# Performance work log

Measured on AMD Instinct MI355X. Metric: run time of the kernel, lower is better.

## Reference

```python
import jax, jax.numpy as jnp
import numpy as np


def setup_inputs() -> dict:
    key = jax.random.key(0)
    k0, k1, k2, k3 = jax.random.split(key, 4)
    B, T, D, F, E = 4, 2048, 512, 1024, 8
    x = jax.random.normal(k0, (B, T, D), dtype=jnp.float32)
    # router weight is zero-init in the original; use small random values so top-k
    router_w = 0.02 * jax.random.normal(k1, (E, D), dtype=jnp.float32)
    router_b = jnp.zeros((E,), dtype=jnp.float32)
    w_gate_up = 0.02 * jax.random.normal(k2, (E, D, 2 * F), dtype=jnp.float32)
    w_down = 0.02 * jax.random.normal(k3, (E, F, D), dtype=jnp.float32)
    return {"x": x, "router_w": router_w, "router_b": router_b,
            "w_gate_up": w_gate_up, "w_down": w_down, "top_k": 2}


def reference(x, router_w, router_b, w_gate_up, w_down, top_k):
    B, T, D = x.shape
    E = router_w.shape[0]
    x_flat = x.reshape(-1, D)                      # [N, D]
    N = x_flat.shape[0]

    # router: softmax over experts, top-k, renormalize
    logits = x_flat @ router_w.T + router_b       # [N, E]
    probs = jax.nn.softmax(logits, axis=-1)
    top_w, top_idx = jax.lax.top_k(probs, top_k)  # [N, k]
    top_w = top_w / jnp.sum(top_w, axis=-1, keepdims=True)

    # scatter renormalized weights into a dense [N, E] combine matrix
    combine = jnp.zeros((N, E), dtype=x.dtype).at[
        jnp.arange(N)[:, None], top_idx].add(top_w)

    # per-expert SwiGLU; combine weights zero out non-selected experts, giving
    # math identical to the sort/gather/scatter dispatch in the original
    out = jnp.zeros_like(x_flat)
    for e in range(E):  # fixed small expert count, not a data-dim loop
        gate_up = x_flat @ w_gate_up[e]           # [N, 2F]
        gate, up = jnp.split(gate_up, 2, axis=-1)
        h = jax.nn.silu(gate) * up                # [N, F]
        out = out + combine[:, e:e + 1] * (h @ w_down[e])
    return out.reshape(B, T, D)
```

## Files before the change

kernel.cpp:

```cpp
#include <hip/hip_runtime.h>
#include <stdint.h>

#define N_TOK 8192
#define D_DIM 512
#define F_DIM 1024
#define E_NUM 8
#define M_SLOTS (N_TOK * 2)

typedef __bf16 bf16x8 __attribute__((ext_vector_type(8)));
typedef float f32x4 __attribute__((ext_vector_type(4)));

__device__ __forceinline__ ushort f2b(float f) {
    union { float f; unsigned u; } v; v.f = f;
    unsigned r = v.u + 0x7fffu + ((v.u >> 16) & 1u);
    return (ushort)(r >> 16);
}
__device__ __forceinline__ float b2f(ushort u) {
    union { unsigned i; float f; } v; v.i = ((unsigned)u) << 16; return v.f;
}
__device__ __forceinline__ void gload16(const void* g, void* l) {
    __builtin_amdgcn_global_load_lds(
        (const __attribute__((address_space(1))) unsigned int*)g,
        (__attribute__((address_space(3))) unsigned int*)l, 16, 0, 0);
}

__global__ __launch_bounds__(256) void pre_k(const float* __restrict__ x,
                                             const float* __restrict__ rw,
                                             const float* __restrict__ rb,
                                             ushort* __restrict__ x_bf,
                                             int* __restrict__ tok_e,
                                             float* __restrict__ tok_w,
                                             int* __restrict__ cnt,
                                             const float* __restrict__ wgu,
                                             ushort* __restrict__ wgu_t,
                                             const float* __restrict__ wd,
                                             ushort* __restrict__ wd_t) {
    __shared__ ushort tile[64][65];
    int b = blockIdx.x;
    if (b < N_TOK / 4) {
        if (b == 0 && threadIdx.x < 16) cnt[threadIdx.x] = 0;
        int lane = threadIdx.x & 63, wv = threadIdx.x >> 6;
        int t = b * 4 + wv;
        float4 xa = *(const float4*)(x + (size_t)t * D_DIM + lane * 8);
        float4 xb = *(const float4*)(x + (size_t)t * D_DIM + lane * 8 + 4);
        ushort u[8] = {f2b(xa.x), f2b(xa.y), f2b(xa.z), f2b(xa.w),
                       f2b(xb.x), f2b(xb.y), f2b(xb.z), f2b(xb.w)};
        *(uint4*)(x_bf + (size_t)t * D_DIM + lane * 8) = *(const uint4*)u;

        float acc[E_NUM];
#pragma unroll
        for (int e = 0; e < E_NUM; ++e) {
            float4 wa = *(const float4*)(rw + (size_t)e * D_DIM + lane * 8);
            float4 wb = *(const float4*)(rw + (size_t)e * D_DIM + lane * 8 + 4);
            float s = xa.x * wa.x + xa.y * wa.y + xa.z * wa.z + xa.w * wa.w +
                      xb.x * wb.x + xb.y * wb.y + xb.z * wb.z + xb.w * wb.w;
#pragma unroll
            for (int o = 32; o > 0; o >>= 1) s += __shfl_xor(s, o, 64);
            acc[e] = s;
        }
        if (lane == 0) {
            float l[E_NUM];
#pragma unroll
            for (int e = 0; e < E_NUM; ++e) l[e] = acc[e] + rb[e];
            int e0 = 0;
#pragma unroll
            for (int e = 1; e < E_NUM; ++e) if (l[e] > l[e0]) e0 = e;
            int e1 = (e0 == 0) ? 1 : 0;
#pragma unroll
            for (int e = 0; e < E_NUM; ++e) if (e != e0 && l[e] > l[e1]) e1 = e;
            float p1 = __expf(l[e1] - l[e0]);
            float w0 = 1.f / (1.f + p1), w1 = p1 / (1.f + p1);
            tok_e[2 * t] = e0;  tok_e[2 * t + 1] = e1;
            tok_w[2 * t] = w0;  tok_w[2 * t + 1] = w1;
        }
        return;
    }
    int tb = b - N_TOK / 4;
    const float* src; ushort* dst; int R, C, c0, r0;
    if (tb < 2048) {
        int e = tb >> 8, rem = tb & 255;
        R = D_DIM; C = 2 * F_DIM;
        src = wgu + (size_t)e * R * C; dst = wgu_t + (size_t)e * R * C;
        c0 = (rem & 31) * 64; r0 = (rem >> 5) * 64;
    } else {
        int b2 = tb - 2048;
        int e = b2 >> 7, rem = b2 & 127;
        R = F_DIM; C = D_DIM;
        src = wd + (size_t)e * R * C; dst = wd_t + (size_t)e * R * C;
        c0 = (rem & 7) * 64; r0 = (rem >> 3) * 64;
    }
#pragma unroll
    for (int i = 0; i < 4; ++i) {
        int ch = threadIdx.x + i * 256;
        int row = ch >> 4, pos = ch & 15;
        float4 v = *(const float4*)(src + (size_t)(r0 + row) * C + c0 + pos * 4);
        tile[row][pos * 4 + 0] = f2b(v.x);
        tile[row][pos * 4 + 1] = f2b(v.y);
        tile[row][pos * 4 + 2] = f2b(v.z);
        tile[row][pos * 4 + 3] = f2b(v.w);
    }
    __syncthreads();
#pragma unroll
    for (int i = 0; i < 2; ++i) {
        int ch = threadIdx.x + i * 256;
        int ocol = ch >> 3, rb_ = ch & 7;
        ushort tmp[8];
#pragma unroll
        for (int j = 0; j < 8; ++j) tmp[j] = tile[rb_ * 8 + j][ocol];
        *(uint4*)(dst + (size_t)(c0 + ocol) * R + r0 + rb_ * 8) = *(const uint4*)tmp;
    }
}

__global__ __launch_bounds__(256) void assign_k(const int* __restrict__ tok_e,
                                                int* __restrict__ cnt,
                                                int* __restrict__ rank) {
    __shared__ int lcnt[E_NUM], lbase[E_NUM];
    int tid = threadIdx.x;
    int i = blockIdx.x * 256 + tid;
    if (tid < E_NUM) lcnt[tid] = 0;
    __syncthreads();
    int e = tok_e[i];
    int intra = atomicAdd(&lcnt[e], 1);
    __syncthreads();
    if (tid < E_NUM) lbase[tid] = atomicAdd(&cnt[tid], lcnt[tid]);
    __syncthreads();
    rank[i] = lbase[e] + intra;
}

__global__ __launch_bounds__(256) void scatter_k(const int* __restrict__ tok_e,
                                                 const int* __restrict__ rank,
                                                 const int* __restrict__ cnt,
                                                 int* __restrict__ ebase,
                                                 int* __restrict__ row_token,
                                                 int* __restrict__ tok_pos) {
    __shared__ int eb[E_NUM];
    int tid = threadIdx.x;
    if (tid == 0) {
        int s = 0;
        for (int k = 0; k < E_NUM; ++k) {
            eb[k] = s;
            if (blockIdx.x == 0) ebase[k] = s;
            s += cnt[k];
        }
        if (blockIdx.x == 0) ebase[E_NUM] = s;
    }
    __syncthreads();
    int i = blockIdx.x * 256 + tid;
    int pos = eb[tok_e[i]] + rank[i];
    row_token[pos] = i >> 1;
    tok_pos[i] = pos;
}

__global__ __launch_bounds__(256, 3) void gemm1_k(const ushort* __restrict__ x,
                                                  const ushort* __restrict__ wgu_t,
                                                  const int* __restrict__ ebase,
                                                  const int* __restrict__ row_token,
                                                  ushort* __restrict__ h) {
    int e = blockIdx.z;
    int base = ebase[e];
    int cnt = ebase[e + 1] - base;
    int tile0 = blockIdx.y * 128;
    if (tile0 >= cnt) return;
    int c0 = blockIdx.x * 64;

    __shared__ __align__(16) ushort smem[3 * 8192];

    int tid = threadIdx.x;
    int lane = tid & 63, wv = tid >> 6;
    int wr = wv >> 1, wc = wv & 1;

    const ushort* asrc[2];
    const ushort* bsrc[2];
#pragma unroll
    for (int i = 0; i < 2; ++i) {
        int c = tid + i * 256;
        int rp = c >> 3, s = c & 7;
        int lp = s ^ (rp & 7);
        int row = 2 * rp + (lp >> 2);
        int q = lp & 3;
        int r = tile0 + row;
        r = (r < cnt) ? r : (cnt - 1);
        int tok = row_token[base + r];
        asrc[i] = x + (size_t)tok * D_DIM + q * 8;
        int gc = (row < 64) ? (c0 + row) : (F_DIM + c0 + row - 64);
        bsrc[i] = wgu_t + ((size_t)e * (2 * F_DIM) + gc) * D_DIM + q * 8;
    }

    f32x4 accg[4][2], accu[4][2];
#pragma unroll
    for (int a = 0; a < 4; ++a)
#pragma unroll
        for (int b = 0; b < 2; ++b) {
            accg[a][b] = (f32x4){0.f, 0.f, 0.f, 0.f};
            accu[a][b] = (f32x4){0.f, 0.f, 0.f, 0.f};
        }

    int q = lane >> 4, m = lane & 15;
    int mh = m >> 1;
    int sl = (4 * (m & 1) + q) ^ (mh & 7);
    int soff = sl * 8;

    auto stage = [&](ushort* buf, int kk) {
#pragma unroll
        for (int i = 0; i < 2; ++i) {
            int c = tid + i * 256;
            gload16(asrc[i] + kk, buf + (size_t)c * 8);
            gload16(bsrc[i] + kk, buf + 4096 + (size_t)c * 8);
        }
    };
    auto compute = [&](const ushort* la_) {
        const ushort* lb_ = la_ + 4096;
        bf16x8 af[4], bg[2], bu[2];
#pragma unroll
        for (int mt = 0; mt < 4; ++mt)
            af[mt] = *(const bf16x8*)(la_ + (wr * 32 + mt * 8 + mh) * 64 + soff);
#pragma unroll
        for (int nt = 0; nt < 2; ++nt) {
            bg[nt] = *(const bf16x8*)(lb_ + (wc * 16 + nt * 8 + mh) * 64 + soff);
            bu[nt] = *(const bf16x8*)(lb_ + (32 + wc * 16 + nt * 8 + mh) * 64 + soff);
        }
#pragma unroll
        for (int mt = 0; mt < 4; ++mt)
#pragma unroll
            for (int nt = 0; nt < 2; ++nt) {
                accg[mt][nt] = __builtin_amdgcn_mfma_f32_16x16x32_bf16(af[mt], bg[nt], accg[mt][nt], 0, 0, 0);
                accu[mt][nt] = __builtin_amdgcn_mfma_f32_16x16x32_bf16(af[mt], bu[nt], accu[mt][nt], 0, 0, 0);
            }
    };

    ushort* pc = smem;
    ushort* pn = smem + 8192;
    ushort* pf = smem + 16384;

    stage(pc, 0);
    stage(pn, 32);
    asm volatile("s_waitcnt vmcnt(4) lgkmcnt(0)" ::: "memory");
    __builtin_amdgcn_s_barrier();
    __builtin_amdgcn_sched_barrier(0);

    for (int k = 64; k <= D_DIM - 32; k += 32) {
        stage(pf, k);
        compute(pc);
        asm volatile("s_waitcnt vmcnt(4) lgkmcnt(0)" ::: "memory");
        __builtin_amdgcn_s_barrier();
        __builtin_amdgcn_sched_barrier(0);
        ushort* t_ = pc; pc = pn; pn = pf; pf = t_;
    }
    compute(pc);
    asm volatile("s_waitcnt vmcnt(0) lgkmcnt(0)" ::: "memory");
    __builtin_amdgcn_s_barrier();
    __builtin_amdgcn_sched_barrier(0);
    compute(pn);

    __syncthreads();
    ushort* stg = smem;
#pragma unroll
    for (int mt = 0; mt < 4; ++mt)
#pragma unroll
        for (int nt = 0; nt < 2; ++nt) {
            int sc = wc * 32 + nt * 16 + m;
#pragma unroll
            for (int r4 = 0; r4 < 4; ++r4) {
                int rr = wr * 64 + mt * 16 + q * 4 + r4;
                float g = accg[mt][nt][r4];
                float u = accu[mt][nt][r4];
                stg[rr * 68 + sc] = f2b((g / (1.f + __expf(-g))) * u);
            }
        }
    __syncthreads();
#pragma unroll
    for (int p = 0; p < 4; ++p) {
        int c = tid + p * 256;
        int sr = c >> 3, coff = (c & 7) * 8;
        int grow = tile0 + sr;
        if (grow < cnt)
            *(uint4*)(h + (size_t)(base + grow) * F_DIM + c0 + coff) =
                *(const uint4*)(stg + sr * 68 + coff);
    }
}

__global__ __launch_bounds__(256, 4) void gemm2_k(const ushort* __restrict__ h,
                                                  const ushort* __restrict__ wd_t,
                                                  const int* __restrict__ ebase,
                                                  ushort* __restrict__ slot) {
    int e = blockIdx.z;
    int base = ebase[e];
    int cnt = ebase[e + 1] - base;
    int tile0 = blockIdx.y * 128;
    if (tile0 >= cnt) return;
    int c0 = blockIdx.x * 64;

    __shared__ __align__(16) ushort smem[3 * 6144];

    int tid = threadIdx.x;
    int lane = tid & 63, wv = tid >> 6;
    int wr = wv >> 1, wc = wv & 1;

    const ushort* asrc[2];
    const ushort* bsrc1;
#pragma unroll
    for (int i = 0; i < 2; ++i) {
        int c = tid + i * 256;
        int rp = c >> 3, s = c & 7;
        int lp = s ^ (rp & 7);
        int row = 2 * rp + (lp >> 2);
        int q = lp & 3;
        int r = tile0 + row;
        r = (r < cnt) ? r : (cnt - 1);
        asrc[i] = h + (size_t)(base + r) * F_DIM + q * 8;
    }
    {
        int c = tid;
        int rp = c >> 3, s = c & 7;
        int lp = s ^ (rp & 7);
        int row = 2 * rp + (lp >> 2);
        int q = lp & 3;
        bsrc1 = wd_t + ((size_t)e * D_DIM + c0 + row) * F_DIM + q * 8;
    }

    f32x4 acc[4][2];
#pragma unroll
    for (int a = 0; a < 4; ++a)
#pragma unroll
        for (int b = 0; b < 2; ++b) acc[a][b] = (f32x4){0.f, 0.f, 0.f, 0.f};

    int q = lane >> 4, m = lane & 15;
    int mh = m >> 1;
    int sl = (4 * (m & 1) + q) ^ (mh & 7);
    int soff = sl * 8;

    auto stage = [&](ushort* buf, int kk) {
#pragma unroll
        for (int i = 0; i < 2; ++i) {
            int c = tid + i * 256;
            gload16(asrc[i] + kk, buf + (size_t)c * 8);
        }
        gload16(bsrc1 + kk, buf + 4096 + (size_t)tid * 8);
    };
    auto compute = [&](const ushort* la_) {
        const ushort* lb_ = la_ + 4096;
        bf16x8 af[4], bb[2];
#pragma unroll
        for (int mt = 0; mt < 4; ++mt)
            af[mt] = *(const bf16x8*)(la_ + (wr * 32 + mt * 8 + mh) * 64 + soff);
#pragma unroll
        for (int nt = 0; nt < 2; ++nt)
            bb[nt] = *(const bf16x8*)(lb_ + (wc * 16 + nt * 8 + mh) * 64 + soff);
#pragma unroll
        for (int mt = 0; mt < 4; ++mt)
#pragma unroll
            for (int nt = 0; nt < 2; ++nt)
                acc[mt][nt] = __builtin_amdgcn_mfma_f32_16x16x32_bf16(af[mt], bb[nt], acc[mt][nt], 0, 0, 0);
    };

    ushort* pc = smem;
    ushort* pn = smem + 6144;
    ushort* pf = smem + 12288;

    stage(pc, 0);
    stage(pn, 32);
    asm volatile("s_waitcnt vmcnt(3) lgkmcnt(0)" ::: "memory");
    __builtin_amdgcn_s_barrier();
    __builtin_amdgcn_sched_barrier(0);

    for (int k = 64; k <= F_DIM - 32; k += 32) {
        stage(pf, k);
        compute(pc);
        asm volatile("s_waitcnt vmcnt(3) lgkmcnt(0)" ::: "memory");
        __builtin_amdgcn_s_barrier();
        __builtin_amdgcn_sched_barrier(0);
        ushort* t_ = pc; pc = pn; pn = pf; pf = t_;
    }
    compute(pc);
    asm volatile("s_waitcnt vmcnt(0) lgkmcnt(0)" ::: "memory");
    __builtin_amdgcn_s_barrier();
    __builtin_amdgcn_sched_barrier(0);
    compute(pn);

    __syncthreads();
    ushort* stg = smem;
#pragma unroll
    for (int mt = 0; mt < 4; ++mt)
#pragma unroll
        for (int nt = 0; nt < 2; ++nt) {
            int sc = wc * 32 + nt * 16 + m;
#pragma unroll
            for (int r4 = 0; r4 < 4; ++r4) {
                int rr = wr * 64 + mt * 16 + q * 4 + r4;
                stg[rr * 68 + sc] = f2b(acc[mt][nt][r4]);
            }
        }
    __syncthreads();
#pragma unroll
    for (int p = 0; p < 4; ++p) {
        int c = tid + p * 256;
        int sr = c >> 3, coff = (c & 7) * 8;
        int grow = tile0 + sr;
        if (grow < cnt)
            *(uint4*)(slot + (size_t)(base + grow) * D_DIM + c0 + coff) =
                *(const uint4*)(stg + sr * 68 + coff);
    }
}

__global__ __launch_bounds__(256) void combine_k(const ushort* __restrict__ slot,
                                                 const int* __restrict__ tok_pos,
                                                 const float* __restrict__ tok_w,
                                                 float* __restrict__ out) {
    int lane = threadIdx.x & 63, wv = threadIdx.x >> 6;
    int t = blockIdx.x * 4 + wv;
    int p0 = tok_pos[2 * t], p1 = tok_pos[2 * t + 1];
    float w0 = tok_w[2 * t], w1 = tok_w[2 * t + 1];
    uint4 s0 = *(const uint4*)(slot + (size_t)p0 * D_DIM + lane * 8);
    uint4 s1 = *(const uint4*)(slot + (size_t)p1 * D_DIM + lane * 8);
    const ushort* a = (const ushort*)&s0;
    const ushort* b = (const ushort*)&s1;
    float o[8];
#pragma unroll
    for (int j = 0; j < 8; ++j) o[j] = w0 * b2f(a[j]) + w1 * b2f(b[j]);
    float* dst = out + (size_t)t * D_DIM + lane * 8;
    *(float4*)dst = (float4){o[0], o[1], o[2], o[3]};
    *(float4*)(dst + 4) = (float4){o[4], o[5], o[6], o[7]};
}

extern "C" void kernel_launch(void* const* d_in, const int* in_sizes, int n_in,
                              void* d_out, int out_size, void* d_ws, size_t ws_size,
                              hipStream_t stream) {
    const float* x   = (const float*)d_in[0];
    const float* rw  = (const float*)d_in[1];
    const float* rb  = (const float*)d_in[2];
    const float* wgu = (const float*)d_in[3];
    const float* wd  = (const float*)d_in[4];
    float* out = (float*)d_out;

    char* ws = (char*)d_ws;
    size_t off = 0;
    auto alloc = [&](size_t bytes) -> void* {
        void* p = ws + off;
        off += (bytes + 255) & ~(size_t)255;
        return p;
    };
    ushort* wgu_t     = (ushort*)alloc((size_t)E_NUM * 2 * F_DIM * D_DIM * 2);
    ushort* wd_t      = (ushort*)alloc((size_t)E_NUM * D_DIM * F_DIM * 2);
    ushort* x_bf      = (ushort*)alloc((size_t)N_TOK * D_DIM * 2);
    ushort* hbuf      = (ushort*)alloc((size_t)M_SLOTS * F_DIM * 2);
    ushort* slot      = (ushort*)alloc((size_t)M_SLOTS * D_DIM * 2);
    int*    row_token = (int*)alloc(M_SLOTS * 4);
    int*    tok_e     = (int*)alloc(M_SLOTS * 4);
    int*    rankbuf   = (int*)alloc(M_SLOTS * 4);
    float*  tok_w     = (float*)alloc(M_SLOTS * 4);
    int*    tok_pos   = (int*)alloc(M_SLOTS * 4);
    int*    cnt       = (int*)alloc(64);
    int*    ebase     = (int*)alloc(64);

    pre_k<<<N_TOK / 4 + 3072, 256, 0, stream>>>(x, rw, rb, x_bf, tok_e, tok_w, cnt,
                                                wgu, wgu_t, wd, wd_t);
    assign_k<<<M_SLOTS / 256, 256, 0, stream>>>(tok_e, cnt, rankbuf);
    scatter_k<<<M_SLOTS / 256, 256, 0, stream>>>(tok_e, rankbuf, cnt, ebase, row_token, tok_pos);
    gemm1_k<<<dim3(16, 32, E_NUM), 256, 0, stream>>>(x_bf, wgu_t, ebase, row_token, hbuf);
    gemm2_k<<<dim3(8, 32, E_NUM), 256, 0, stream>>>(hbuf, wd_t, ebase, slot);
    combine_k<<<N_TOK / 4, 256, 0, stream>>>(slot, tok_pos, tok_w, out);
}
```

Before: 219.2 us.

## Fuse combine into down-projection GEMM epilogue via atomic scatter-add

Removes the separate combine kernel and the bf16 slot buffer. The down-projection GEMM now scales its outputs by the routing weight and atomically adds them into the fp32 output, which the pre-kernel zero-initialises. The GEMM2 tile is widened to 128 columns, with four N sub-tiles per wave and MFMA priority hints. The cost is 16K×512 scalar float atomics, and the summation order between the two experts becomes nondeterministic.

Measured after the change: 419.6 us. 91.5% more time.

```diff
diff --git a/kernel.cpp b/kernel.cpp
--- a/kernel.cpp
+++ b/kernel.cpp
@@ -34,13 +34,17 @@
                                              const float* __restrict__ wgu,
                                              ushort* __restrict__ wgu_t,
                                              const float* __restrict__ wd,
-                                             ushort* __restrict__ wd_t) {
+                                             ushort* __restrict__ wd_t,
+                                             float* __restrict__ out) {
     __shared__ ushort tile[64][65];
     int b = blockIdx.x;
     if (b < N_TOK / 4) {
         if (b == 0 && threadIdx.x < 16) cnt[threadIdx.x] = 0;
         int lane = threadIdx.x & 63, wv = threadIdx.x >> 6;
         int t = b * 4 + wv;
+        float4 z4 = (float4){0.f, 0.f, 0.f, 0.f};
+        *(float4*)(out + (size_t)t * D_DIM + lane * 8) = z4;
+        *(float4*)(out + (size_t)t * D_DIM + lane * 8 + 4) = z4;
         float4 xa = *(const float4*)(x + (size_t)t * D_DIM + lane * 8);
         float4 xb = *(const float4*)(x + (size_t)t * D_DIM + lane * 8 + 4);
         ushort u[8] = {f2b(xa.x), f2b(xa.y), f2b(xa.z), f2b(xa.w),
@@ -131,8 +135,7 @@
                                                  const int* __restrict__ rank,
                                                  const int* __restrict__ cnt,
                                                  int* __restrict__ ebase,
-                                                 int* __restrict__ row_token,
-                                                 int* __restrict__ tok_pos) {
+                                                 int* __restrict__ row_token) {
     __shared__ int eb[E_NUM];
     int tid = threadIdx.x;
     if (tid == 0) {
@@ -147,8 +150,7 @@
     __syncthreads();
     int i = blockIdx.x * 256 + tid;
     int pos = eb[tok_e[i]] + rank[i];
-    row_token[pos] = i >> 1;
-    tok_pos[i] = pos;
+    row_token[pos] = i;
 }
 
 __global__ __launch_bounds__(256, 3) void gemm1_k(const ushort* __restrict__ x,
@@ -180,7 +182,7 @@
         int q = lp & 3;
         int r = tile0 + row;
         r = (r < cnt) ? r : (cnt - 1);
-        int tok = row_token[base + r];
+        int tok = row_token[base + r] >> 1;
         asrc[i] = x + (size_t)tok * D_DIM + q * 8;
         int gc = (row < 64) ? (c0 + row) : (F_DIM + c0 + row - 64);
         bsrc[i] = wgu_t + ((size_t)e * (2 * F_DIM) + gc) * D_DIM + q * 8;
@@ -279,25 +281,26 @@
     }
 }
 
-__global__ __launch_bounds__(256, 4) void gemm2_k(const ushort* __restrict__ h,
+__global__ __launch_bounds__(256, 3) void gemm2_k(const ushort* __restrict__ h,
                                                   const ushort* __restrict__ wd_t,
                                                   const int* __restrict__ ebase,
-                                                  ushort* __restrict__ slot) {
+                                                  const int* __restrict__ row_token,
+                                                  const float* __restrict__ tok_w,
+                                                  float* __restrict__ out) {
     int e = blockIdx.z;
     int base = ebase[e];
     int cnt = ebase[e + 1] - base;
     int tile0 = blockIdx.y * 128;
     if (tile0 >= cnt) return;
-    int c0 = blockIdx.x * 64;
-
-    __shared__ __align__(16) ushort smem[3 * 6144];
+    int c0 = blockIdx.x * 128;
+
+    __shared__ __align__(16) ushort smem[3 * 8192];
 
     int tid = threadIdx.x;
     int lane = tid & 63, wv = tid >> 6;
     int wr = wv >> 1, wc = wv & 1;
 
-    const ushort* asrc[2];
-    const ushort* bsrc1;
+    const ushort* asrc[2]; const ushort* bsrc[2];
 #pragma unroll
     for (int i = 0; i < 2; ++i) {
         int c = tid + i * 256;
@@ -308,21 +311,14 @@
         int r = tile0 + row;
         r = (r < cnt) ? r : (cnt - 1);
         asrc[i] = h + (size_t)(base + r) * F_DIM + q * 8;
-    }
-    {
-        int c = tid;
-        int rp = c >> 3, s = c & 7;
-        int lp = s ^ (rp & 7);
-        int row = 2 * rp + (lp >> 2);
-        int q = lp & 3;
-        bsrc1 = wd_t + ((size_t)e * D_DIM + c0 + row) * F_DIM + q * 8;
-    }
-
-    f32x4 acc[4][2];
+        bsrc[i] = wd_t + ((size_t)e * D_DIM + c0 + row) * F_DIM + q * 8;
+    }
+
+    f32x4 acc[4][4];
 #pragma unroll
     for (int a = 0; a < 4; ++a)
 #pragma unroll
-        for (int b = 0; b < 2; ++b) acc[a][b] = (f32x4){0.f, 0.f, 0.f, 0.f};
+        for (int b = 0; b < 4; ++b) acc[a][b] = (f32x4){0.f, 0.f, 0.f, 0.f};
 
     int q = lane >> 4, m = lane & 15;
     int mh = m >> 1;
@@ -334,39 +330,41 @@
         for (int i = 0; i < 2; ++i) {
             int c = tid + i * 256;
             gload16(asrc[i] + kk, buf + (size_t)c * 8);
-        }
-        gload16(bsrc1 + kk, buf + 4096 + (size_t)tid * 8);
+            gload16(bsrc[i] + kk, buf + 4096 + (size_t)c * 8);
+        }
     };
     auto compute = [&](const ushort* la_) {
         const ushort* lb_ = la_ + 4096;
-        bf16x8 af[4], bb[2];
+        bf16x8 af[4], bb[4];
 #pragma unroll
         for (int mt = 0; mt < 4; ++mt)
             af[mt] = *(const bf16x8*)(la_ + (wr * 32 + mt * 8 + mh) * 64 + soff);
 #pragma unroll
-        for (int nt = 0; nt < 2; ++nt)
-            bb[nt] = *(const bf16x8*)(lb_ + (wc * 16 + nt * 8 + mh) * 64 + soff);
+        for (int nt = 0; nt < 4; ++nt)
+            bb[nt] = *(const bf16x8*)(lb_ + (wc * 32 + nt * 8 + mh) * 64 + soff);
+        __builtin_amdgcn_s_setprio(1);
 #pragma unroll
         for (int mt = 0; mt < 4; ++mt)
 #pragma unroll
-            for (int nt = 0; nt < 2; ++nt)
+            for (int nt = 0; nt < 4; ++nt)
                 acc[mt][nt] = __builtin_amdgcn_mfma_f32_16x16x32_bf16(af[mt], bb[nt], acc[mt][nt], 0, 0, 0);
+        __builtin_amdgcn_s_setprio(0);
     };
 
     ushort* pc = smem;
-    ushort* pn = smem + 6144;
-    ushort* pf = smem + 12288;
+    ushort* pn = smem + 8192;
+    ushort* pf = smem + 16384;
 
     stage(pc, 0);
     stage(pn, 32);
-    asm volatile("s_waitcnt vmcnt(3) lgkmcnt(0)" ::: "memory");
+    asm volatile("s_waitcnt vmcnt(4) lgkmcnt(0)" ::: "memory");
     __builtin_amdgcn_s_barrier();
     __builtin_amdgcn_sched_barrier(0);
 
     for (int k = 64; k <= F_DIM - 32; k += 32) {
         stage(pf, k);
         compute(pc);
-        asm volatile("s_waitcnt vmcnt(3) lgkmcnt(0)" ::: "memory");
+        asm volatile("s_waitcnt vmcnt(4) lgkmcnt(0)" ::: "memory");
         __builtin_amdgcn_s_barrier();
         __builtin_amdgcn_sched_barrier(0);
         ushort* t_ = pc; pc = pn; pn = pf; pf = t_;
@@ -382,44 +380,31 @@
 #pragma unroll
     for (int mt = 0; mt < 4; ++mt)
 #pragma unroll
-        for (int nt = 0; nt < 2; ++nt) {
-            int sc = wc * 32 + nt * 16 + m;
+        for (int nt = 0; nt < 4; ++nt) {
+            int scol = wc * 64 + nt * 16 + m;
 #pragma unroll
             for (int r4 = 0; r4 < 4; ++r4) {
                 int rr = wr * 64 + mt * 16 + q * 4 + r4;
-                stg[rr * 68 + sc] = f2b(acc[mt][nt][r4]);
+                stg[rr * 132 + scol] = f2b(acc[mt][nt][r4]);
             }
         }
     __syncthreads();
 #pragma unroll
-    for (int p = 0; p < 4; ++p) {
+    for (int p = 0; p < 8; ++p) {
         int c = tid + p * 256;
-        int sr = c >> 3, coff = (c & 7) * 8;
+        int sr = c >> 4, coff = (c & 15) * 8;
         int grow = tile0 + sr;
-        if (grow < cnt)
-            *(uint4*)(slot + (size_t)(base + grow) * D_DIM + c0 + coff) =
-                *(const uint4*)(stg + sr * 68 + coff);
-    }
-}
-
-__global__ __launch_bounds__(256) void combine_k(const ushort* __restrict__ slot,
-                                                 const int* __restrict__ tok_pos,
-                                                 const float* __restrict__ tok_w,
-                                                 float* __restrict__ out) {
-    int lane = threadIdx.x & 63, wv = threadIdx.x >> 6;
-    int t = blockIdx.x * 4 + wv;
-    int p0 = tok_pos[2 * t], p1 = tok_pos[2 * t + 1];
-    float w0 = tok_w[2 * t], w1 = tok_w[2 * t + 1];
-    uint4 s0 = *(const uint4*)(slot + (size_t)p0 * D_DIM + lane * 8);
-    uint4 s1 = *(const uint4*)(slot + (size_t)p1 * D_DIM + lane * 8);
-    const ushort* a = (const ushort*)&s0;
-    const ushort* b = (const ushort*)&s1;
-    float o[8];
-#pragma unroll
-    for (int j = 0; j < 8; ++j) o[j] = w0 * b2f(a[j]) + w1 * b2f(b[j]);
-    float* dst = out + (size_t)t * D_DIM + lane * 8;
-    *(float4*)dst = (float4){o[0], o[1], o[2], o[3]};
-    *(float4*)(dst + 4) = (float4){o[4], o[5], o[6], o[7]};
+        if (grow < cnt) {
+            int s_  = row_token[base + grow];
+            int tok = s_ >> 1;
+            float w = tok_w[s_];
+            const ushort* sp = stg + sr * 132 + coff;
+            float* dst = out + (size_t)tok * D_DIM + c0 + coff;
+#pragma unroll
+            for (int j = 0; j < 8; ++j)
+                atomicAdd(dst + j, w * b2f(sp[j]));
+        }
+    }
 }
 
 extern "C" void kernel_launch(void* const* d_in, const int* in_sizes, int n_in,
@@ -443,20 +428,17 @@
     ushort* wd_t      = (ushort*)alloc((size_t)E_NUM * D_DIM * F_DIM * 2);
     ushort* x_bf      = (ushort*)alloc((size_t)N_TOK * D_DIM * 2);
     ushort* hbuf      = (ushort*)alloc((size_t)M_SLOTS * F_DIM * 2);
-    ushort* slot      = (ushort*)alloc((size_t)M_SLOTS * D_DIM * 2);
     int*    row_token = (int*)alloc(M_SLOTS * 4);
     int*    tok_e     = (int*)alloc(M_SLOTS * 4);
     int*    rankbuf   = (int*)alloc(M_SLOTS * 4);
     float*  tok_w     = (float*)alloc(M_SLOTS * 4);
-    int*    tok_pos   = (int*)alloc(M_SLOTS * 4);
     int*    cnt       = (int*)alloc(64);
     int*    ebase     = (int*)alloc(64);
 
     pre_k<<<N_TOK / 4 + 3072, 256, 0, stream>>>(x, rw, rb, x_bf, tok_e, tok_w, cnt,
-                                                wgu, wgu_t, wd, wd_t);
+                                                wgu, wgu_t, wd, wd_t, out);
     assign_k<<<M_SLOTS / 256, 256, 0, stream>>>(tok_e, cnt, rankbuf);
-    scatter_k<<<M_SLOTS / 256, 256, 0, stream>>>(tok_e, rankbuf, cnt, ebase, row_token, tok_pos);
+    scatter_k<<<M_SLOTS / 256, 256, 0, stream>>>(tok_e, rankbuf, cnt, ebase, row_token);
     gemm1_k<<<dim3(16, 32, E_NUM), 256, 0, stream>>>(x_bf, wgu_t, ebase, row_token, hbuf);
-    gemm2_k<<<dim3(8, 32, E_NUM), 256, 0, stream>>>(hbuf, wd_t, ebase, slot);
-    combine_k<<<N_TOK / 4, 256, 0, stream>>>(slot, tok_pos, tok_w, out);
-}
+    gemm2_k<<<dim3(4, 32, E_NUM), 256, 0, stream>>>(hbuf, wd_t, ebase, row_token, tok_w, out);
+}
```
